# Kernel tuning notes

Measured on AMD Instinct MI355X. Metric: run time of the kernel, lower is better.

## Reference

```python
import jax, jax.numpy as jnp
import numpy as np

N_WIN = 7    # n_win hardcoded in AR_Attention
TOPK = 4     # topk routing windows
HEADS = 8    # num_heads


def setup_inputs() -> dict:
    key = jax.random.key(0)
    ks = jax.random.split(key, 6)
    B, H, W, C = 4, 56, 56, 256
    s = 0.02
    x = jax.random.normal(ks[0], (B, H, W, C), jnp.float32)
    Wqkv = jax.random.normal(ks[1], (C, 3 * C), jnp.float32) * s  # Linear(dim, 3*dim) (qk_dim=dim)
    bqkv = jnp.zeros((3 * C,), jnp.float32)
    Wo = jax.random.normal(ks[2], (C, C), jnp.float32) * s        # output projection Linear(dim, dim)
    bo = jnp.zeros((C,), jnp.float32)
    lepe_w = jax.random.normal(ks[3], (5, 5, 1, C), jnp.float32) * s  # 5x5 depthwise conv (side_dwconv=5)
    lepe_b = jnp.zeros((C,), jnp.float32)
    return {"x": x, "Wqkv": Wqkv, "bqkv": bqkv, "Wo": Wo, "bo": bo,
            "lepe_w": lepe_w, "lepe_b": lepe_b}


def reference(x, Wqkv, bqkv, Wo, bo, lepe_w, lepe_b):
    B, H, W, C = x.shape
    nw = N_WIN
    h, w = H // nw, W // nw           # region size (8x8)
    p2 = nw * nw                      # number of regions (49)
    hd = C // HEADS                   # head dim
    scale = float(C) ** -0.5          # qk_scale = qk_dim ** -0.5 (qk_dim = dim)

    # region partition: [B,H,W,C] -> [B,p2,h,w,C]
    xr = x.reshape(B, nw, h, nw, w, C).transpose(0, 1, 3, 2, 4, 5).reshape(B, p2, h, w, C)

    qkv = xr @ Wqkv + bqkv            # [B,p2,h,w,3C]
    q, kv = qkv[..., :C], qkv[..., C:]

    q_pix = q.reshape(B, p2, h * w, C)
    kv_pix = kv.reshape(B, p2, h * w, 2 * C)   # kv_downsample_mode='identity'

    # region-level queries/keys via per-window mean pooling
    q_win = q.mean((2, 3))                     # [B,p2,C]
    k_win = kv[..., :C].mean((2, 3))           # [B,p2,C]

    # LEPE: 5x5 depthwise conv on v over the full image grid
    v_img = kv[..., C:].reshape(B, nw, nw, h, w, C).transpose(0, 1, 3, 2, 4, 5).reshape(B, H, W, C)
    lepe = jax.lax.conv_general_dilated(
        v_img, lepe_w, (1, 1), 'SAME',
        dimension_numbers=('NHWC', 'HWIO', 'NHWC'),
        feature_group_count=C) + lepe_b

    # top-k window routing (param_routing=False, hard routing, mul_weight='none')
    r_logit = jnp.einsum('bpc,bqc->bpq', q_win * scale, k_win)  # [B,p2,p2]
    _, r_idx = jax.lax.top_k(r_logit, TOPK)                     # [B,p2,TOPK]

    # gather selected kv windows: [B,p2,TOPK,h*w,2C]
    kv_sel = jax.vmap(lambda kvp, i: kvp[i])(kv_pix, r_idx)

    k_sel = kv_sel[..., :C].reshape(B, p2, TOPK * h * w, HEADS, hd)
    v_sel = kv_sel[..., C:].reshape(B, p2, TOPK * h * w, HEADS, hd)
    qh = q_pix.reshape(B, p2, h * w, HEADS, hd)

    attn = jnp.einsum('bpqnd,bpknd->bpnqk', qh * scale, k_sel)  # [B,p2,heads,hw,TOPK*hw]
    attn = jax.nn.softmax(attn, axis=-1)
    out = jnp.einsum('bpnqk,bpknd->bpqnd', attn, v_sel).reshape(B, p2, h, w, C)

    # windows back to image grid
    out = out.reshape(B, nw, nw, h, w, C).transpose(0, 1, 3, 2, 4, 5).reshape(B, H, W, C)
    out = out + lepe
    return out @ Wo + bo
```

## Files before the change

kernel.cpp:

```cpp
#include <hip/hip_runtime.h>
#include <hip/hip_bf16.h>

#define NPIX 12544

typedef short bf16x8 __attribute__((ext_vector_type(8)));
typedef short bf16x4 __attribute__((ext_vector_type(4)));
typedef float f32x4  __attribute__((ext_vector_type(4)));

__device__ __forceinline__ float bf2f(unsigned short u) {
    unsigned int x = ((unsigned int)u) << 16;
    float f; __builtin_memcpy(&f, &x, sizeof(f)); return f;
}
__device__ __forceinline__ unsigned short f2bf(float f) {
    __hip_bfloat16 h = __float2bfloat16(f);
    unsigned short u; __builtin_memcpy(&u, &h, 2); return u;
}
__device__ __forceinline__ void load_lds16(const unsigned short* g, unsigned short* l) {
    __builtin_amdgcn_global_load_lds(
        (const __attribute__((address_space(1))) unsigned int*)g,
        (__attribute__((address_space(3))) unsigned int*)l,
        16, 0, 0);
}
__device__ __forceinline__ unsigned ldsoff(const void* p) {
    return (unsigned)(unsigned long long)(const __attribute__((address_space(3))) char*)p;
}
template<int OFF>
__device__ __forceinline__ bf16x4 tr16(unsigned addr) {
    bf16x4 d;
    asm volatile("ds_read_b64_tr_b16 %0, %1 offset:%c2"
                 : "=v"(d) : "v"(addr), "i"(OFF));
    return d;
}

__global__ __launch_bounds__(256) void k_prep(
    const float* __restrict__ X, unsigned short* __restrict__ Xb,
    float* __restrict__ xmean,
    const float* __restrict__ Wqkv, const float* __restrict__ Wo,
    unsigned short* __restrict__ Wtq, unsigned short* __restrict__ Wto)
{
    __shared__ __align__(16) unsigned char sm[64 * 65 * 4];
    const int t = threadIdx.x;
    const int blk = blockIdx.x;
    if (blk < 392) {
        float* part = (float*)sm;
        const int w = blk >> 1, hc = blk & 1;
        const int b = w / 49, p = w % 49;
        const int wi = p / 7, wj = p % 7;
        const int ch0 = hc * 128;
        const int ps = t >> 5, cg = t & 31;
        float4 s = {0.f, 0.f, 0.f, 0.f};
        #pragma unroll
        for (int i = 0; i < 8; i++) {
            int pp = ps * 8 + i;
            int y = wi * 8 + (pp >> 3), x = wj * 8 + (pp & 7);
            int idx = (((b * 56) + y) * 56 + x) * 256 + ch0 + cg * 4;
            float4 v = *reinterpret_cast<const float4*>(X + idx);
            s.x += v.x; s.y += v.y; s.z += v.z; s.w += v.w;
            ushort4 o = { f2bf(v.x), f2bf(v.y), f2bf(v.z), f2bf(v.w) };
            *reinterpret_cast<ushort4*>(Xb + idx) = o;
        }
        *reinterpret_cast<float4*>(part + t * 4) = *reinterpret_cast<float4*>(&s);
        __syncthreads();
        if (t < 32) {
            float4 m = {0.f, 0.f, 0.f, 0.f};
            #pragma unroll
            for (int ps2 = 0; ps2 < 8; ps2++) {
                float4 v = *reinterpret_cast<float4*>(part + (ps2 * 32 + t) * 4);
                m.x += v.x; m.y += v.y; m.z += v.z; m.w += v.w;
            }
            m.x *= (1.f / 64.f); m.y *= (1.f / 64.f);
            m.z *= (1.f / 64.f); m.w *= (1.f / 64.f);
            *reinterpret_cast<float4*>(xmean + w * 256 + ch0 + t * 4) = m;
        }
    } else {
        float* tile = (float*)sm;
        int tb = blk - 392;
        const float* Wsrc; unsigned short* Wdst; int N, kt, nt;
        if (tb < 48) { Wsrc = Wqkv; Wdst = Wtq; N = 768; kt = tb / 12; nt = tb % 12; }
        else { tb -= 48; Wsrc = Wo; Wdst = Wto; N = 256; kt = tb / 4; nt = tb % 4; }
        const int k0 = kt * 64, n0 = nt * 64;
        const int r0 = t >> 6, c = t & 63;
        #pragma unroll
        for (int i = 0; i < 16; i++) {
            int r = i * 4 + r0;
            tile[r * 65 + c] = Wsrc[(size_t)(k0 + r) * N + n0 + c];
        }
        __syncthreads();
        #pragma unroll
        for (int i = 0; i < 16; i++) {
            int n = i * 4 + r0;
            Wdst[(size_t)(n0 + n) * 256 + k0 + c] = f2bf(tile[c * 65 + n]);
        }
    }
}

__global__ __launch_bounds__(256) void k_main1(
    const unsigned short* __restrict__ A,
    const unsigned short* __restrict__ Bt,
    const float* __restrict__ bias,
    unsigned short* __restrict__ O,
    const float* __restrict__ xmean,
    const float* __restrict__ Wqkv,
    float* __restrict__ qwin, float* __restrict__ kwin)
{
    __shared__ __align__(16) unsigned char sm1[16384];
    const int t = threadIdx.x;
    const int blk = blockIdx.x;
    if (blk < 588) {
        unsigned short* As = (unsigned short*)sm1;
        unsigned short* Bs = (unsigned short*)(sm1 + 8192);
        const int m0 = (blk % 98) * 128, n0 = (blk / 98) * 128;
        const int wave = t >> 6, lane = t & 63, quad = lane >> 4, lo = lane & 15;
        const int wm = wave & 1, wn = wave >> 1;
        const int sr = wave * 16 + (lane >> 2);
        const int sc = lane & 3;
        f32x4 acc[4][4];
        #pragma unroll
        for (int i = 0; i < 4; i++)
            #pragma unroll
            for (int j = 0; j < 4; j++) acc[i][j] = (f32x4){0.f, 0.f, 0.f, 0.f};

        for (int kt = 0; kt < 256; kt += 32) {
            __syncthreads();
            #pragma unroll
            for (int j = 0; j < 2; j++) {
                int row = j * 64 + sr;
                int e = sc ^ ((row >> 1) & 3);
                load_lds16(A  + (size_t)(m0 + row) * 256 + kt + e * 8, &As[row * 32 + sc * 8]);
                load_lds16(Bt + (size_t)(n0 + row) * 256 + kt + e * 8, &Bs[row * 32 + sc * 8]);
            }
            __syncthreads();
            bf16x8 af[4], bfr[4];
            #pragma unroll
            for (int mt = 0; mt < 4; mt++) {
                int row = wm * 64 + mt * 16 + lo;
                int c = quad ^ ((row >> 1) & 3);
                af[mt] = *reinterpret_cast<const bf16x8*>(&As[row * 32 + c * 8]);
            }
            #pragma unroll
            for (int nt = 0; nt < 4; nt++) {
                int col = wn * 64 + nt * 16 + lo;
                int c = quad ^ ((col >> 1) & 3);
                bfr[nt] = *reinterpret_cast<const bf16x8*>(&Bs[col * 32 + c * 8]);
            }
            #pragma unroll
            for (int mt = 0; mt < 4; mt++)
                #pragma unroll
                for (int nt = 0; nt < 4; nt++)
                    acc[mt][nt] = __builtin_amdgcn_mfma_f32_16x16x32_bf16(
                        af[mt], bfr[nt], acc[mt][nt], 0, 0, 0);
        }
        float bv[4];
        #pragma unroll
        for (int nt = 0; nt < 4; nt++) bv[nt] = bias[n0 + wn * 64 + nt * 16 + lo];
        #pragma unroll
        for (int mt = 0; mt < 4; mt++)
            #pragma unroll
            for (int nt = 0; nt < 4; nt++) {
                int n = n0 + wn * 64 + nt * 16 + lo;
                #pragma unroll
                for (int r = 0; r < 4; r++) {
                    int m = m0 + wm * 64 + mt * 16 + quad * 4 + r;
                    O[m * 768 + n] = f2bf(acc[mt][nt][r] + bv[nt]);
                }
            }
    } else {
        float* xs = (float*)sm1;
        const int u = blk - 588;
        const int bp = u % 196;
        const int half = u / 196;
        const int c = t;
        xs[c] = xmean[bp * 256 + c];
        __syncthreads();
        const int col = half * 256 + c;
        float a = 0.f;
        for (int k = 0; k < 256; k++) a += xs[k] * Wqkv[k * 768 + col];
        float* outp = half ? kwin : qwin;
        outp[bp * 256 + c] = a + bias[col];
    }
}

__global__ __launch_bounds__(256) void k_main2(
    const float* __restrict__ qwin, const float* __restrict__ kwin,
    int* __restrict__ ridx,
    const unsigned short* __restrict__ QKV,
    const float* __restrict__ lw, const float* __restrict__ lb,
    unsigned short* __restrict__ Olepe)
{
    __shared__ __align__(16) unsigned char sm2[25600];
    const int t = threadIdx.x;
    const int blk = blockIdx.x;
    if (blk < 196) {
        float* part = (float*)sm2;
        float* lg   = (float*)(sm2 + 49 * 4 * 4);
        const int b = blk / 49, p = blk % 49;
        if (t < 196) {
            int d = t >> 2, pr = t & 3;
            const float* qp = &qwin[(b * 49 + p) * 256];
            const float* kp = &kwin[(b * 49 + d) * 256];
            float a = 0.f;
            for (int ch = pr * 64; ch < pr * 64 + 64; ch++) a += qp[ch] * kp[ch];
            part[d * 4 + pr] = a;
        }
        __syncthreads();
        if (t < 49) lg[t] = part[t * 4 + 0] + part[t * 4 + 1] + part[t * 4 + 2] + part[t * 4 + 3];
        __syncthreads();
        if (t == 0) {
            unsigned long long used = 0ull;
            for (int sel = 0; sel < 4; sel++) {
                float best = -1e30f; int bi = 0;
                for (int qq = 0; qq < 49; qq++)
                    if (!((used >> qq) & 1ull) && lg[qq] > best) { best = lg[qq]; bi = qq; }
                used |= (1ull << bi);
                ridx[blk * 4 + sel] = bi;
            }
        }
    } else {
        float* lws = (float*)sm2;
        #pragma unroll
        for (int i = 0; i < 25; i++) lws[i * 256 + t] = lw[i * 256 + t];

        const int pl = t & 7;
        const int cg = t >> 3;
        const int c0 = cg * 8;
        const int gid = (blk - 196) * 8 + pl;
        const int b = gid / 3136, rem = gid % 3136;
        const int y = rem / 56, x = rem % 56;
        __syncthreads();

        float acc[8];
        {
            float4 b0 = *reinterpret_cast<const float4*>(lb + c0);
            float4 b1 = *reinterpret_cast<const float4*>(lb + c0 + 4);
            acc[0] = b0.x; acc[1] = b0.y; acc[2] = b0.z; acc[3] = b0.w;
            acc[4] = b1.x; acc[5] = b1.y; acc[6] = b1.z; acc[7] = b1.w;
        }
        #pragma unroll
        for (int ky = 0; ky < 5; ky++) {
            int yy = y + ky - 2;
            if (yy < 0 || yy >= 56) continue;
            #pragma unroll
            for (int kx = 0; kx < 5; kx++) {
                int xx = x + kx - 2;
                if (xx < 0 || xx >= 56) continue;
                bf16x8 v = *reinterpret_cast<const bf16x8*>(
                    QKV + (((b * 56) + yy) * 56 + xx) * 768 + 512 + c0);
                const float* wrow = &lws[(ky * 5 + kx) * 256 + c0];
                float4 w0 = *reinterpret_cast<const float4*>(wrow);
                float4 w1 = *reinterpret_cast<const float4*>(wrow + 4);
                acc[0] += bf2f((unsigned short)v[0]) * w0.x;
                acc[1] += bf2f((unsigned short)v[1]) * w0.y;
                acc[2] += bf2f((unsigned short)v[2]) * w0.z;
                acc[3] += bf2f((unsigned short)v[3]) * w0.w;
                acc[4] += bf2f((unsigned short)v[4]) * w1.x;
                acc[5] += bf2f((unsigned short)v[5]) * w1.y;
                acc[6] += bf2f((unsigned short)v[6]) * w1.z;
                acc[7] += bf2f((unsigned short)v[7]) * w1.w;
            }
        }
        bf16x8 o;
        #pragma unroll
        for (int j = 0; j < 8; j++) o[j] = (short)f2bf(acc[j]);
        *reinterpret_cast<bf16x8*>(Olepe + (size_t)gid * 256 + c0) = o;
    }
}

__global__ __launch_bounds__(256) void k_attn(
    const unsigned short* __restrict__ QKV,
    const int* __restrict__ ridx,
    const unsigned short* __restrict__ Olepe,
    unsigned short* __restrict__ Osum)
{
    __shared__ __align__(16) unsigned char smem[53248];
    unsigned short* Vs  = (unsigned short*)smem;
    unsigned short* Qs  = (unsigned short*)(smem + 16384);
    unsigned short* Ks  = (unsigned short*)(smem + 21504);
    unsigned short* PST = (unsigned short*)(smem + 16384);
    unsigned short* OsT = (unsigned short*)(smem + 49152);

    const int p = blockIdx.x, head = blockIdx.y, b = blockIdx.z;
    const int t = threadIdx.x;
    const int wi = p / 7, wj = p % 7;
    const int wave = t >> 6, lane = t & 63, quad = lane >> 4, lo = lane & 15;
    const int pix4 = t >> 2, c4 = t & 3;

    {
        int y = wi * 8 + (pix4 >> 3), x = wj * 8 + (pix4 & 7);
        const unsigned short* qp = QKV + (((b * 56) + y) * 56 + x) * 768 + head * 32 + c4 * 8;
        bf16x8 v = *reinterpret_cast<const bf16x8*>(qp);
        int sw = c4 ^ ((pix4 >> 3) & 3);
        *reinterpret_cast<bf16x8*>(&Qs[pix4 * 40 + sw * 8]) = v;
    }
    #pragma unroll
    for (int pass = 0; pass < 4; pass++) {
        int sel = ridx[(b * 49 + p) * 4 + pass];
        int si = sel / 7, sj = sel % 7;
        int y = si * 8 + (pix4 >> 3), x = sj * 8 + (pix4 & 7);
        const unsigned short* base = QKV + (((b * 56) + y) * 56 + x) * 768 + 256 + head * 32;
        bf16x8 kv = *reinterpret_cast<const bf16x8*>(base + c4 * 8);
        bf16x8 vv = *reinterpret_cast<const bf16x8*>(base + 256 + c4 * 8);
        int krow = pass * 64 + pix4;
        int sw = c4 ^ ((krow >> 3) & 3);
        *reinterpret_cast<bf16x8*>(&Ks[krow * 40 + sw * 8]) = kv;
        *reinterpret_cast<bf16x8*>(
            &Vs[(krow >> 2) * 128 + (c4 >> 1) * 64 + (krow & 3) * 16 + (c4 & 1) * 8]) = vv;
    }
    __syncthreads();

    f32x4 sc[16];
    {
        int row = wave * 16 + lo;
        bf16x8 af = *reinterpret_cast<const bf16x8*>(
            &Qs[row * 40 + ((quad ^ ((row >> 3) & 3)) * 8)]);
        f32x4 z = (f32x4){0.f, 0.f, 0.f, 0.f};
        #pragma unroll
        for (int nt = 0; nt < 16; nt++) {
            int key = nt * 16 + lo;
            bf16x8 bfr = *reinterpret_cast<const bf16x8*>(
                &Ks[key * 40 + ((quad ^ ((key >> 3) & 3)) * 8)]);
            sc[nt] = __builtin_amdgcn_mfma_f32_16x16x32_bf16(af, bfr, z, 0, 0, 0);
        }
    }
    float M[4] = {-1e30f, -1e30f, -1e30f, -1e30f};
    #pragma unroll
    for (int nt = 0; nt < 16; nt++)
        #pragma unroll
        for (int r = 0; r < 4; r++) M[r] = fmaxf(M[r], sc[nt][r] * 0.0625f);
    #pragma unroll
    for (int d = 1; d < 16; d <<= 1)
        #pragma unroll
        for (int r = 0; r < 4; r++) M[r] = fmaxf(M[r], __shfl_xor(M[r], d));
    float l[4] = {0.f, 0.f, 0.f, 0.f};
    #pragma unroll
    for (int nt = 0; nt < 16; nt++)
        #pragma unroll
        for (int r = 0; r < 4; r++) {
            float e = __expf(sc[nt][r] * 0.0625f - M[r]);
            sc[nt][r] = e;
            l[r] += e;
        }
    #pragma unroll
    for (int d = 1; d < 16; d <<= 1)
        #pragma unroll
        for (int r = 0; r < 4; r++) l[r] += __shfl_xor(l[r], d);

    __syncthreads();

    unsigned short* myP = PST + wave * 4096;
    #pragma unroll
    for (int nt = 0; nt < 16; nt++) {
        ushort4 pk = { f2bf(sc[nt][0]), f2bf(sc[nt][1]),
                       f2bf(sc[nt][2]), f2bf(sc[nt][3]) };
        *reinterpret_cast<ushort4*>(&myP[(nt * 16 + lo) * 16 + quad * 4]) = pk;
    }
    const unsigned paddr = ldsoff(myP) + quad * 256 + lo * 8;
    const unsigned vaddr = ldsoff(Vs)  + quad * 512 + lo * 8;
    asm volatile("s_waitcnt lgkmcnt(0)" ::: "memory");
    __builtin_amdgcn_sched_barrier(0);

    bf16x4 ra0, ra1, rw00, rw01, rw10, rw11;
    ra0  = tr16<0>(paddr);
    ra1  = tr16<128>(paddr);
    rw00 = tr16<0>(vaddr);
    rw01 = tr16<256>(vaddr);
    rw10 = tr16<128>(vaddr);
    rw11 = tr16<384>(vaddr);
    f32x4 o0 = (f32x4){0.f, 0.f, 0.f, 0.f}, o1 = o0;
    #pragma unroll
    for (int kt = 0; kt < 8; kt++) {
        bf16x4 na0, na1, nw00, nw01, nw10, nw11;
        if (kt < 7) {
            unsigned pn = paddr + (kt + 1) * 1024;
            unsigned vn = vaddr + (kt + 1) * 2048;
            na0  = tr16<0>(pn);
            na1  = tr16<128>(pn);
            nw00 = tr16<0>(vn);
            nw01 = tr16<256>(vn);
            nw10 = tr16<128>(vn);
            nw11 = tr16<384>(vn);
            asm volatile("s_waitcnt lgkmcnt(6)" ::: "memory");
        } else {
            asm volatile("s_waitcnt lgkmcnt(0)" ::: "memory");
        }
        __builtin_amdgcn_sched_barrier(0);
        bf16x8 pa, vb0, vb1;
        #pragma unroll
        for (int j = 0; j < 4; j++) {
            pa[j]  = ra0[j];  pa[4 + j]  = ra1[j];
            vb0[j] = rw00[j]; vb0[4 + j] = rw01[j];
            vb1[j] = rw10[j]; vb1[4 + j] = rw11[j];
        }
        o0 = __builtin_amdgcn_mfma_f32_16x16x32_bf16(pa, vb0, o0, 0, 0, 0);
        o1 = __builtin_amdgcn_mfma_f32_16x16x32_bf16(pa, vb1, o1, 0, 0, 0);
        if (kt < 7) { ra0 = na0; ra1 = na1; rw00 = nw00; rw01 = nw01; rw10 = nw10; rw11 = nw11; }
    }

    {
        unsigned short* ow = OsT + wave * 512;
        float i0 = 1.f / l[0], i1 = 1.f / l[1], i2 = 1.f / l[2], i3 = 1.f / l[3];
        ushort4 p0 = { f2bf(o0[0] * i0), f2bf(o0[1] * i1),
                       f2bf(o0[2] * i2), f2bf(o0[3] * i3) };
        ushort4 p1 = { f2bf(o1[0] * i0), f2bf(o1[1] * i1),
                       f2bf(o1[2] * i2), f2bf(o1[3] * i3) };
        *reinterpret_cast<ushort4*>(&ow[lo * 16 + quad * 4]) = p0;
        *reinterpret_cast<ushort4*>(&ow[(16 + lo) * 16 + quad * 4]) = p1;
    }
    const unsigned oaddr = ldsoff(OsT) + wave * 1024 + quad * 256 + lo * 8;
    asm volatile("s_waitcnt lgkmcnt(0)" ::: "memory");
    __builtin_amdgcn_sched_barrier(0);
    bf16x4 e0 = tr16<0>(oaddr);
    bf16x4 e1 = tr16<128>(oaddr);
    asm volatile("s_waitcnt lgkmcnt(0)" ::: "memory");
    __builtin_amdgcn_sched_barrier(0);
    {
        int q = wave * 16 + lo;
        int y = wi * 8 + (q >> 3), x = wj * 8 + (q & 7);
        size_t gbase = (size_t)(((b * 56) + y) * 56 + x) * 256 + head * 32 + quad * 8;
        bf16x8 lp = *reinterpret_cast<const bf16x8*>(Olepe + gbase);
        bf16x8 oo;
        #pragma unroll
        for (int j = 0; j < 4; j++) {
            oo[j]     = (short)f2bf(bf2f((unsigned short)e0[j]) + bf2f((unsigned short)lp[j]));
            oo[4 + j] = (short)f2bf(bf2f((unsigned short)e1[j]) + bf2f((unsigned short)lp[4 + j]));
        }
        *reinterpret_cast<bf16x8*>(Osum + gbase) = oo;
    }
}

__global__ __launch_bounds__(256) void k_proj(
    const unsigned short* __restrict__ A,
    const unsigned short* __restrict__ Bt,
    const float* __restrict__ bias,
    float* __restrict__ O)
{
    __shared__ unsigned short As[128 * 32];
    __shared__ unsigned short Bs[64 * 32];
    const int t = threadIdx.x;
    const int m0 = blockIdx.x * 128, n0 = blockIdx.y * 64;
    const int wave = t >> 6, lane = t & 63, quad = lane >> 4, lo = lane & 15;
    const int sr = wave * 16 + (lane >> 2);
    const int sc = lane & 3;
    f32x4 acc[2][4];
    #pragma unroll
    for (int i = 0; i < 2; i++)
        #pragma unroll
        for (int j = 0; j < 4; j++) acc[i][j] = (f32x4){0.f, 0.f, 0.f, 0.f};

    for (int kt = 0; kt < 256; kt += 32) {
        __syncthreads();
        #pragma unroll
        for (int j = 0; j < 2; j++) {
            int row = j * 64 + sr;
            int e = sc ^ ((row >> 1) & 3);
            load_lds16(A + (size_t)(m0 + row) * 256 + kt + e * 8, &As[row * 32 + sc * 8]);
        }
        {
            int e = sc ^ ((sr >> 1) & 3);
            load_lds16(Bt + (size_t)(n0 + sr) * 256 + kt + e * 8, &Bs[sr * 32 + sc * 8]);
        }
        __syncthreads();
        bf16x8 af[2], bfr[4];
        #pragma unroll
        for (int mt = 0; mt < 2; mt++) {
            int row = wave * 32 + mt * 16 + lo;
            int c = quad ^ ((row >> 1) & 3);
            af[mt] = *reinterpret_cast<const bf16x8*>(&As[row * 32 + c * 8]);
        }
        #pragma unroll
        for (int nt = 0; nt < 4; nt++) {
            int col = nt * 16 + lo;
            int c = quad ^ ((col >> 1) & 3);
            bfr[nt] = *reinterpret_cast<const bf16x8*>(&Bs[col * 32 + c * 8]);
        }
        #pragma unroll
        for (int mt = 0; mt < 2; mt++)
            #pragma unroll
            for (int nt = 0; nt < 4; nt++)
                acc[mt][nt] = __builtin_amdgcn_mfma_f32_16x16x32_bf16(
                    af[mt], bfr[nt], acc[mt][nt], 0, 0, 0);
    }
    float bv[4];
    #pragma unroll
    for (int nt = 0; nt < 4; nt++) bv[nt] = bias[n0 + nt * 16 + lo];
    #pragma unroll
    for (int mt = 0; mt < 2; mt++)
        #pragma unroll
        for (int nt = 0; nt < 4; nt++) {
            int n = n0 + nt * 16 + lo;
            #pragma unroll
            for (int r = 0; r < 4; r++) {
                int m = m0 + wave * 32 + mt * 16 + quad * 4 + r;
                O[m * 256 + n] = acc[mt][nt][r] + bv[nt];
            }
        }
}

extern "C" void kernel_launch(void* const* d_in, const int* in_sizes, int n_in,
                              void* d_out, int out_size, void* d_ws, size_t ws_size,
                              hipStream_t stream)
{
    const float* x    = (const float*)d_in[0];
    const float* Wqkv = (const float*)d_in[1];
    const float* bqkv = (const float*)d_in[2];
    const float* Wo   = (const float*)d_in[3];
    const float* bo   = (const float*)d_in[4];
    const float* lw   = (const float*)d_in[5];
    const float* lb   = (const float*)d_in[6];
    float* out = (float*)d_out;

    char* ws = (char*)d_ws;
    size_t off = 0;
    unsigned short* qkv   = (unsigned short*)(ws + off); off += (size_t)NPIX * 768 * 2;
    unsigned short* xb    = (unsigned short*)(ws + off); off += (size_t)NPIX * 256 * 2;
    unsigned short* Wtq   = (unsigned short*)(ws + off); off += 768 * 256 * 2;
    unsigned short* Wto   = (unsigned short*)(ws + off); off += 256 * 256 * 2;
    unsigned short* Osum  = (unsigned short*)(ws + off); off += (size_t)NPIX * 256 * 2;
    unsigned short* Olepe = (unsigned short*)(ws + off); off += (size_t)NPIX * 256 * 2;
    float* xmean = (float*)(ws + off); off += 196 * 256 * 4;
    float* qwin  = (float*)(ws + off); off += 196 * 256 * 4;
    float* kwin  = (float*)(ws + off); off += 196 * 256 * 4;
    int*   ridx  = (int*)(ws + off);   off += 196 * 4 * 4;

    k_prep <<<dim3(456),      256, 0, stream>>>(x, xb, xmean, Wqkv, Wo, Wtq, Wto);
    k_main1<<<dim3(980),      256, 0, stream>>>(xb, Wtq, bqkv, qkv, xmean, Wqkv, qwin, kwin);
    k_main2<<<dim3(1764),     256, 0, stream>>>(qwin, kwin, ridx, qkv, lw, lb, Olepe);
    k_attn <<<dim3(49, 8, 4), 256, 0, stream>>>(qkv, ridx, Olepe, Osum);
    k_proj <<<dim3(98, 4),    256, 0, stream>>>(Osum, Wto, bo, out);
}
```

Before: 154.5 us.

## Fuse LEPE depthwise conv into attention kernel and double-buffer GEMM LDS loads

Moves the 5x5 depthwise LEPE convolution out of k_main2 into the attention kernel, computed per head in registers with weights staged in LDS. This drops the Olepe intermediate buffer and its global write and read. It also double-buffers the LDS tiles in the QKV and output projection GEMMs using vmcnt waits and raw barriers, so global-to-LDS loads overlap MFMA compute. The cost is more LDS use in the GEMMs, extra register pressure and scattered global reads in the attention kernel, and O staging now reuses the P buffer region.

```diff
diff --git a/kernel.cpp b/kernel.cpp
--- a/kernel.cpp
+++ b/kernel.cpp
@@ -103,12 +103,12 @@
     const float* __restrict__ Wqkv,
     float* __restrict__ qwin, float* __restrict__ kwin)
 {
-    __shared__ __align__(16) unsigned char sm1[16384];
+    __shared__ __align__(16) unsigned char sm1[32768];
     const int t = threadIdx.x;
     const int blk = blockIdx.x;
     if (blk < 588) {
         unsigned short* As = (unsigned short*)sm1;
-        unsigned short* Bs = (unsigned short*)(sm1 + 8192);
+        unsigned short* Bs = (unsigned short*)(sm1 + 16384);
         const int m0 = (blk % 98) * 128, n0 = (blk / 98) * 128;
         const int wave = t >> 6, lane = t & 63, quad = lane >> 4, lo = lane & 15;
         const int wm = wave & 1, wn = wave >> 1;
@@ -120,28 +120,41 @@
             #pragma unroll
             for (int j = 0; j < 4; j++) acc[i][j] = (f32x4){0.f, 0.f, 0.f, 0.f};
 
-        for (int kt = 0; kt < 256; kt += 32) {
-            __syncthreads();
+        auto stage = [&](int it) {
+            int kt = it * 32;
+            unsigned short* Ad = As + (it & 1) * 4096;
+            unsigned short* Bd = Bs + (it & 1) * 4096;
             #pragma unroll
             for (int j = 0; j < 2; j++) {
                 int row = j * 64 + sr;
                 int e = sc ^ ((row >> 1) & 3);
-                load_lds16(A  + (size_t)(m0 + row) * 256 + kt + e * 8, &As[row * 32 + sc * 8]);
-                load_lds16(Bt + (size_t)(n0 + row) * 256 + kt + e * 8, &Bs[row * 32 + sc * 8]);
-            }
-            __syncthreads();
+                load_lds16(A  + (size_t)(m0 + row) * 256 + kt + e * 8, &Ad[row * 32 + sc * 8]);
+                load_lds16(Bt + (size_t)(n0 + row) * 256 + kt + e * 8, &Bd[row * 32 + sc * 8]);
+            }
+        };
+        stage(0);
+        for (int it = 0; it < 8; ++it) {
+            if (it < 7) {
+                stage(it + 1);
+                asm volatile("s_waitcnt vmcnt(4)" ::: "memory");
+            } else {
+                asm volatile("s_waitcnt vmcnt(0)" ::: "memory");
+            }
+            __builtin_amdgcn_s_barrier();
+            const unsigned short* Ac = As + (it & 1) * 4096;
+            const unsigned short* Bc = Bs + (it & 1) * 4096;
             bf16x8 af[4], bfr[4];
             #pragma unroll
             for (int mt = 0; mt < 4; mt++) {
                 int row = wm * 64 + mt * 16 + lo;
                 int c = quad ^ ((row >> 1) & 3);
-                af[mt] = *reinterpret_cast<const bf16x8*>(&As[row * 32 + c * 8]);
+                af[mt] = *reinterpret_cast<const bf16x8*>(&Ac[row * 32 + c * 8]);
             }
             #pragma unroll
             for (int nt = 0; nt < 4; nt++) {
                 int col = wn * 64 + nt * 16 + lo;
                 int c = quad ^ ((col >> 1) & 3);
-                bfr[nt] = *reinterpret_cast<const bf16x8*>(&Bs[col * 32 + c * 8]);
+                bfr[nt] = *reinterpret_cast<const bf16x8*>(&Bc[col * 32 + c * 8]);
             }
             #pragma unroll
             for (int mt = 0; mt < 4; mt++)
@@ -149,6 +162,7 @@
                 for (int nt = 0; nt < 4; nt++)
                     acc[mt][nt] = __builtin_amdgcn_mfma_f32_16x16x32_bf16(
                         af[mt], bfr[nt], acc[mt][nt], 0, 0, 0);
+            __builtin_amdgcn_s_barrier();
         }
         float bv[4];
         #pragma unroll
@@ -182,101 +196,49 @@
 
 __global__ __launch_bounds__(256) void k_main2(
     const float* __restrict__ qwin, const float* __restrict__ kwin,
-    int* __restrict__ ridx,
-    const unsigned short* __restrict__ QKV,
-    const float* __restrict__ lw, const float* __restrict__ lb,
-    unsigned short* __restrict__ Olepe)
+    int* __restrict__ ridx)
 {
-    __shared__ __align__(16) unsigned char sm2[25600];
+    __shared__ __align__(16) unsigned char sm2[1024];
     const int t = threadIdx.x;
     const int blk = blockIdx.x;
-    if (blk < 196) {
-        float* part = (float*)sm2;
-        float* lg   = (float*)(sm2 + 49 * 4 * 4);
-        const int b = blk / 49, p = blk % 49;
-        if (t < 196) {
-            int d = t >> 2, pr = t & 3;
-            const float* qp = &qwin[(b * 49 + p) * 256];
-            const float* kp = &kwin[(b * 49 + d) * 256];
-            float a = 0.f;
-            for (int ch = pr * 64; ch < pr * 64 + 64; ch++) a += qp[ch] * kp[ch];
-            part[d * 4 + pr] = a;
-        }
-        __syncthreads();
-        if (t < 49) lg[t] = part[t * 4 + 0] + part[t * 4 + 1] + part[t * 4 + 2] + part[t * 4 + 3];
-        __syncthreads();
-        if (t == 0) {
-            unsigned long long used = 0ull;
-            for (int sel = 0; sel < 4; sel++) {
-                float best = -1e30f; int bi = 0;
-                for (int qq = 0; qq < 49; qq++)
-                    if (!((used >> qq) & 1ull) && lg[qq] > best) { best = lg[qq]; bi = qq; }
-                used |= (1ull << bi);
-                ridx[blk * 4 + sel] = bi;
-            }
-        }
-    } else {
-        float* lws = (float*)sm2;
-        #pragma unroll
-        for (int i = 0; i < 25; i++) lws[i * 256 + t] = lw[i * 256 + t];
-
-        const int pl = t & 7;
-        const int cg = t >> 3;
-        const int c0 = cg * 8;
-        const int gid = (blk - 196) * 8 + pl;
-        const int b = gid / 3136, rem = gid % 3136;
-        const int y = rem / 56, x = rem % 56;
-        __syncthreads();
-
-        float acc[8];
-        {
-            float4 b0 = *reinterpret_cast<const float4*>(lb + c0);
-            float4 b1 = *reinterpret_cast<const float4*>(lb + c0 + 4);
-            acc[0] = b0.x; acc[1] = b0.y; acc[2] = b0.z; acc[3] = b0.w;
-            acc[4] = b1.x; acc[5] = b1.y; acc[6] = b1.z; acc[7] = b1.w;
-        }
-        #pragma unroll
-        for (int ky = 0; ky < 5; ky++) {
-            int yy = y + ky - 2;
-            if (yy < 0 || yy >= 56) continue;
-            #pragma unroll
-            for (int kx = 0; kx < 5; kx++) {
-                int xx = x + kx - 2;
-                if (xx < 0 || xx >= 56) continue;
-                bf16x8 v = *reinterpret_cast<const bf16x8*>(
-                    QKV + (((b * 56) + yy) * 56 + xx) * 768 + 512 + c0);
-                const float* wrow = &lws[(ky * 5 + kx) * 256 + c0];
-                float4 w0 = *reinterpret_cast<const float4*>(wrow);
-                float4 w1 = *reinterpret_cast<const float4*>(wrow + 4);
-                acc[0] += bf2f((unsigned short)v[0]) * w0.x;
-                acc[1] += bf2f((unsigned short)v[1]) * w0.y;
-                acc[2] += bf2f((unsigned short)v[2]) * w0.z;
-                acc[3] += bf2f((unsigned short)v[3]) * w0.w;
-                acc[4] += bf2f((unsigned short)v[4]) * w1.x;
-                acc[5] += bf2f((unsigned short)v[5]) * w1.y;
-                acc[6] += bf2f((unsigned short)v[6]) * w1.z;
-                acc[7] += bf2f((unsigned short)v[7]) * w1.w;
-            }
-        }
-        bf16x8 o;
-        #pragma unroll
-        for (int j = 0; j < 8; j++) o[j] = (short)f2bf(acc[j]);
-        *reinterpret_cast<bf16x8*>(Olepe + (size_t)gid * 256 + c0) = o;
+    float* part = (float*)sm2;
+    float* lg   = (float*)(sm2 + 49 * 4 * 4);
+    const int b = blk / 49, p = blk % 49;
+    if (t < 196) {
+        int d = t >> 2, pr = t & 3;
+        const float* qp = &qwin[(b * 49 + p) * 256];
+        const float* kp = &kwin[(b * 49 + d) * 256];
+        float a = 0.f;
+        for (int ch = pr * 64; ch < pr * 64 + 64; ch++) a += qp[ch] * kp[ch];
+        part[d * 4 + pr] = a;
+    }
+    __syncthreads();
+    if (t < 49) lg[t] = part[t * 4 + 0] + part[t * 4 + 1] + part[t * 4 + 2] + part[t * 4 + 3];
+    __syncthreads();
+    if (t == 0) {
+        unsigned long long used = 0ull;
+        for (int sel = 0; sel < 4; sel++) {
+            float best = -1e30f; int bi = 0;
+            for (int qq = 0; qq < 49; qq++)
+                if (!((used >> qq) & 1ull) && lg[qq] > best) { best = lg[qq]; bi = qq; }
+            used |= (1ull << bi);
+            ridx[blk * 4 + sel] = bi;
+        }
     }
 }
 
 __global__ __launch_bounds__(256) void k_attn(
     const unsigned short* __restrict__ QKV,
     const int* __restrict__ ridx,
-    const unsigned short* __restrict__ Olepe,
+    const float* __restrict__ lw, const float* __restrict__ lb,
     unsigned short* __restrict__ Osum)
 {
-    __shared__ __align__(16) unsigned char smem[53248];
+    __shared__ __align__(16) unsigned char smem[52352];
     unsigned short* Vs  = (unsigned short*)smem;
     unsigned short* Qs  = (unsigned short*)(smem + 16384);
     unsigned short* Ks  = (unsigned short*)(smem + 21504);
     unsigned short* PST = (unsigned short*)(smem + 16384);
-    unsigned short* OsT = (unsigned short*)(smem + 49152);
+    float* lws          = (float*)(smem + 49152);
 
     const int p = blockIdx.x, head = blockIdx.y, b = blockIdx.z;
     const int t = threadIdx.x;
@@ -284,6 +246,11 @@
     const int wave = t >> 6, lane = t & 63, quad = lane >> 4, lo = lane & 15;
     const int pix4 = t >> 2, c4 = t & 3;
 
+    if (t < 200) {
+        int tap = t >> 3, ci = (t & 7) * 4;
+        *reinterpret_cast<float4*>(&lws[tap * 32 + ci]) =
+            *reinterpret_cast<const float4*>(lw + tap * 256 + head * 32 + ci);
+    }
     {
         int y = wi * 8 + (pix4 >> 3), x = wj * 8 + (pix4 & 7);
         const unsigned short* qp = QKV + (((b * 56) + y) * 56 + x) * 768 + head * 32 + c4 * 8;
@@ -306,6 +273,39 @@
             &Vs[(krow >> 2) * 128 + (c4 >> 1) * 64 + (krow & 3) * 16 + (c4 & 1) * 8]) = vv;
     }
     __syncthreads();
+
+    float lep[8];
+    {
+        int q = wave * 16 + lo;
+        int py = wi * 8 + (q >> 3), px = wj * 8 + (q & 7);
+        float4 b0 = *reinterpret_cast<const float4*>(lb + head * 32 + quad * 8);
+        float4 b1 = *reinterpret_cast<const float4*>(lb + head * 32 + quad * 8 + 4);
+        lep[0] = b0.x; lep[1] = b0.y; lep[2] = b0.z; lep[3] = b0.w;
+        lep[4] = b1.x; lep[5] = b1.y; lep[6] = b1.z; lep[7] = b1.w;
+        #pragma unroll
+        for (int ky = 0; ky < 5; ky++) {
+            int yy = py + ky - 2;
+            if (yy < 0 || yy >= 56) continue;
+            #pragma unroll
+            for (int kx = 0; kx < 5; kx++) {
+                int xx = px + kx - 2;
+                if (xx < 0 || xx >= 56) continue;
+                bf16x8 v = *reinterpret_cast<const bf16x8*>(
+                    QKV + (((b * 56) + yy) * 56 + xx) * 768 + 512 + head * 32 + quad * 8);
+                const float* wrow = &lws[(ky * 5 + kx) * 32 + quad * 8];
+                float4 w0 = *reinterpret_cast<const float4*>(wrow);
+                float4 w1 = *reinterpret_cast<const float4*>(wrow + 4);
+                lep[0] += bf2f((unsigned short)v[0]) * w0.x;
+                lep[1] += bf2f((unsigned short)v[1]) * w0.y;
+                lep[2] += bf2f((unsigned short)v[2]) * w0.z;
+                lep[3] += bf2f((unsigned short)v[3]) * w0.w;
+                lep[4] += bf2f((unsigned short)v[4]) * w1.x;
+                lep[5] += bf2f((unsigned short)v[5]) * w1.y;
+                lep[6] += bf2f((unsigned short)v[6]) * w1.z;
+                lep[7] += bf2f((unsigned short)v[7]) * w1.w;
+            }
+        }
+    }
 
     f32x4 sc[16];
     {
@@ -396,7 +396,7 @@
     }
 
     {
-        unsigned short* ow = OsT + wave * 512;
+        unsigned short* ow = myP;
         float i0 = 1.f / l[0], i1 = 1.f / l[1], i2 = 1.f / l[2], i3 = 1.f / l[3];
         ushort4 p0 = { f2bf(o0[0] * i0), f2bf(o0[1] * i1),
                        f2bf(o0[2] * i2), f2bf(o0[3] * i3) };
@@ -405,7 +405,7 @@
         *reinterpret_cast<ushort4*>(&ow[lo * 16 + quad * 4]) = p0;
         *reinterpret_cast<ushort4*>(&ow[(16 + lo) * 16 + quad * 4]) = p1;
     }
-    const unsigned oaddr = ldsoff(OsT) + wave * 1024 + quad * 256 + lo * 8;
+    const unsigned oaddr = ldsoff(PST) + wave * 8192 + quad * 256 + lo * 8;
     asm volatile("s_waitcnt lgkmcnt(0)" ::: "memory");
     __builtin_amdgcn_sched_barrier(0);
     bf16x4 e0 = tr16<0>(oaddr);
@@ -416,12 +416,11 @@
         int q = wave * 16 + lo;
         int y = wi * 8 + (q >> 3), x = wj * 8 + (q & 7);
         size_t gbase = (size_t)(((b * 56) + y) * 56 + x) * 256 + head * 32 + quad * 8;
-        bf16x8 lp = *reinterpret_cast<const bf16x8*>(Olepe + gbase);
         bf16x8 oo;
         #pragma unroll
         for (int j = 0; j < 4; j++) {
-            oo[j]     = (short)f2bf(bf2f((unsigned short)e0[j]) + bf2f((unsigned short)lp[j]));
-            oo[4 + j] = (short)f2bf(bf2f((unsigned short)e1[j]) + bf2f((unsigned short)lp[4 + j]));
+            oo[j]     = (short)f2bf(bf2f((unsigned short)e0[j]) + lep[j]);
+            oo[4 + j] = (short)f2bf(bf2f((unsigned short)e1[j]) + lep[4 + j]);
         }
         *reinterpret_cast<bf16x8*>(Osum + gbase) = oo;
     }
@@ -433,8 +432,8 @@
     const float* __restrict__ bias,
     float* __restrict__ O)
 {
-    __shared__ unsigned short As[128 * 32];
-    __shared__ unsigned short Bs[64 * 32];
+    __shared__ __align__(16) unsigned short As[2 * 128 * 32];
+    __shared__ __align__(16) unsigned short Bs[2 * 64 * 32];
     const int t = threadIdx.x;
     const int m0 = blockIdx.x * 128, n0 = blockIdx.y * 64;
     const int wave = t >> 6, lane = t & 63, quad = lane >> 4, lo = lane & 15;
@@ -446,31 +445,44 @@
         #pragma unroll
         for (int j = 0; j < 4; j++) acc[i][j] = (f32x4){0.f, 0.f, 0.f, 0.f};
 
-    for (int kt = 0; kt < 256; kt += 32) {
-        __syncthreads();
+    auto stage = [&](int it) {
+        int kt = it * 32;
+        unsigned short* Ad = As + (it & 1) * 4096;
+        unsigned short* Bd = Bs + (it & 1) * 2048;
         #pragma unroll
         for (int j = 0; j < 2; j++) {
             int row = j * 64 + sr;
             int e = sc ^ ((row >> 1) & 3);
-            load_lds16(A + (size_t)(m0 + row) * 256 + kt + e * 8, &As[row * 32 + sc * 8]);
+            load_lds16(A + (size_t)(m0 + row) * 256 + kt + e * 8, &Ad[row * 32 + sc * 8]);
         }
         {
             int e = sc ^ ((sr >> 1) & 3);
-            load_lds16(Bt + (size_t)(n0 + sr) * 256 + kt + e * 8, &Bs[sr * 32 + sc * 8]);
-        }
-        __syncthreads();
+            load_lds16(Bt + (size_t)(n0 + sr) * 256 + kt + e * 8, &Bd[sr * 32 + sc * 8]);
+        }
+    };
+    stage(0);
+    for (int it = 0; it < 8; ++it) {
+        if (it < 7) {
+            stage(it + 1);
+            asm volatile("s_waitcnt vmcnt(3)" ::: "memory");
+        } else {
+            asm volatile("s_waitcnt vmcnt(0)" ::: "memory");
+        }
+        __builtin_amdgcn_s_barrier();
+        const unsigned short* Ac = As + (it & 1) * 4096;
+        const unsigned short* Bc = Bs + (it & 1) * 2048;
         bf16x8 af[2], bfr[4];
         #pragma unroll
         for (int mt = 0; mt < 2; mt++) {
             int row = wave * 32 + mt * 16 + lo;
             int c = quad ^ ((row >> 1) & 3);
-            af[mt] = *reinterpret_cast<const bf16x8*>(&As[row * 32 + c * 8]);
+            af[mt] = *reinterpret_cast<const bf16x8*>(&Ac[row * 32 + c * 8]);
         }
         #pragma unroll
         for (int nt = 0; nt < 4; nt++) {
             int col = nt * 16 + lo;
             int c = quad ^ ((col >> 1) & 3);
-            bfr[nt] = *reinterpret_cast<const bf16x8*>(&Bs[col * 32 + c * 8]);
+            bfr[nt] = *reinterpret_cast<const bf16x8*>(&Bc[col * 32 + c * 8]);
         }
         #pragma unroll
         for (int mt = 0; mt < 2; mt++)
@@ -478,6 +490,7 @@
             for (int nt = 0; nt < 4; nt++)
                 acc[mt][nt] = __builtin_amdgcn_mfma_f32_16x16x32_bf16(
                     af[mt], bfr[nt], acc[mt][nt], 0, 0, 0);
+        __builtin_amdgcn_s_barrier();
     }
     float bv[4];
     #pragma unroll
@@ -515,7 +528,6 @@
     unsigned short* Wtq   = (unsigned short*)(ws + off); off += 768 * 256 * 2;
     unsigned short* Wto   = (unsigned short*)(ws + off); off += 256 * 256 * 2;
     unsigned short* Osum  = (unsigned short*)(ws + off); off += (size_t)NPIX * 256 * 2;
-    unsigned short* Olepe = (unsigned short*)(ws + off); off += (size_t)NPIX * 256 * 2;
     float* xmean = (float*)(ws + off); off += 196 * 256 * 4;
     float* qwin  = (float*)(ws + off); off += 196 * 256 * 4;
     float* kwin  = (float*)(ws + off); off += 196 * 256 * 4;
@@ -523,7 +535,7 @@
 
     k_prep <<<dim3(456),      256, 0, stream>>>(x, xb, xmean, Wqkv, Wo, Wtq, Wto);
     k_main1<<<dim3(980),      256, 0, stream>>>(xb, Wtq, bqkv, qkv, xmean, Wqkv, qwin, kwin);
-    k_main2<<<dim3(1764),     256, 0, stream>>>(qwin, kwin, ridx, qkv, lw, lb, Olepe);
-    k_attn <<<dim3(49, 8, 4), 256, 0, stream>>>(qkv, ridx, Olepe, Osum);
+    k_main2<<<dim3(196),      256, 0, stream>>>(qwin, kwin, ridx);
+    k_attn <<<dim3(49, 8, 4), 256, 0, stream>>>(qkv, ridx, lw, lb, Osum);
     k_proj <<<dim3(98, 4),    256, 0, stream>>>(Osum, Wto, bo, out);
 }
```

After: 164.7 us. 1.07x slower.
